# Kernel optimization log

Hardware: AMD Instinct MI355X
Metric: run time of the kernel (lower is better)

The kernel has to match this reference:

```python
import jax, jax.numpy as jnp
import numpy as np

N = 50000      # nodes
E = 800000     # edges (avg degree 16)
F_IN = 3       # dataset.num_node_features
H = 256        # hidden_channels
G = 64         # batch_size (num graphs)
OUT = 24       # lin_out output dim


def setup_inputs() -> dict:
    key = jax.random.key(0)
    ks = jax.random.split(key, 16)
    s = 0.05
    inp = {
        "x": jax.random.normal(ks[0], (N, F_IN), jnp.float32),
        "edge_index": jax.random.randint(ks[1], (2, E), 0, N, dtype=jnp.int32),
        "batch": jnp.sort(jax.random.randint(ks[2], (N,), 0, G, dtype=jnp.int32)),
        # layer 1 (F_IN -> H)
        "w_rel1": jax.random.normal(ks[3], (F_IN, H), jnp.float32) * s,
        "w_root1": jax.random.normal(ks[4], (F_IN, H), jnp.float32) * s,
        "b1": jnp.zeros((H,), jnp.float32),
        # layers 2..7 (H -> H), stacked
        "w_rel": jax.random.normal(ks[5], (6, H, H), jnp.float32) * s,
        "w_root": jax.random.normal(ks[6], (6, H, H), jnp.float32) * s,
        "b": jnp.zeros((6, H), jnp.float32),
        # output head
        "w_out": jax.random.normal(ks[7], (H, OUT), jnp.float32) * s,
        "b_out": jnp.zeros((OUT,), jnp.float32),
    }
    return inp


def reference(x, edge_index, batch, w_rel1, w_root1, b1, w_rel, w_root, b, w_out, b_out):
    src, dst = edge_index[0], edge_index[1]

    def conv(h, wr, wro, bb):
        # PyG GraphConv with add aggregation:
        # out_i = W_rel @ sum_{j -> i} h_j + b + W_root @ h_i
        agg = jax.ops.segment_sum(h[src], dst, num_segments=N)
        return agg @ wr + h @ wro + bb

    h = jax.nn.relu(conv(x, w_rel1, w_root1, b1))
    for i in range(6):
        h = jax.nn.relu(conv(h, w_rel[i], w_root[i], b[i]))

    # global_mean_pool over batch segment ids
    counts = jax.ops.segment_sum(jnp.ones((N,), h.dtype), batch, num_segments=G)
    pooled = jax.ops.segment_sum(h, batch, num_segments=G) / jnp.maximum(counts, 1.0)[:, None]

    # dropout is identity in eval mode
    return pooled @ w_out + b_out
```

## Files before the change

kernel.cpp:

```cpp
#include <hip/hip_runtime.h>

#define N_NODES 50000
#define MPAD 50048
#define N_EDGES 800000
#define H 256
#define K_CAT 512
#define G_BATCH 64
#define OUT_DIM 24

#define SCAN_BLK 256
#define NBLK ((N_NODES + SCAN_BLK - 1) / SCAN_BLK)

typedef __attribute__((ext_vector_type(8))) short short8;
typedef __attribute__((ext_vector_type(4))) float float4v;

__device__ __forceinline__ float bf2f(unsigned short u) {
    return __uint_as_float(((unsigned)u) << 16);
}
__device__ __forceinline__ unsigned short f2bf(float f) {
    unsigned x = __float_as_uint(f);
    unsigned r = (x + 0x7FFFu + ((x >> 16) & 1u)) >> 16;
    return (unsigned short)r;
}

__device__ __forceinline__ void async_copy16(void* lds, const void* g) {
    __builtin_amdgcn_global_load_lds(
        (const __attribute__((address_space(1))) unsigned int*)g,
        (__attribute__((address_space(3))) unsigned int*)lds, 16, 0, 0);
}



__global__ void histo_kernel(const int* __restrict__ dst, int* __restrict__ deg,
                             int* __restrict__ epos) {
    int e = blockIdx.x * blockDim.x + threadIdx.x;
    if (e < N_EDGES) epos[e] = atomicAdd(&deg[dst[e]], 1);
}

__global__ void scan_block(const int* __restrict__ deg, int* __restrict__ rowptr,
                           int* __restrict__ blockSums) {
    __shared__ int s[SCAN_BLK];
    int idx = blockIdx.x * SCAN_BLK + threadIdx.x;
    int v = (idx < N_NODES) ? deg[idx] : 0;
    s[threadIdx.x] = v;
    __syncthreads();
    for (int off = 1; off < SCAN_BLK; off <<= 1) {
        int t = (threadIdx.x >= off) ? s[threadIdx.x - off] : 0;
        __syncthreads();
        s[threadIdx.x] += t;
        __syncthreads();
    }
    if (idx < N_NODES) rowptr[idx] = s[threadIdx.x] - v;
    if (threadIdx.x == SCAN_BLK - 1) blockSums[blockIdx.x] = s[threadIdx.x];
}

__global__ void scan_finish(int* __restrict__ rowptr, const int* __restrict__ blockSums) {
    __shared__ int s[SCAN_BLK];
    int t = threadIdx.x;
    int v = (t < NBLK) ? blockSums[t] : 0;
    s[t] = v;
    __syncthreads();
    for (int off = 1; off < SCAN_BLK; off <<= 1) {
        int tv = (t >= off) ? s[t - off] : 0;
        __syncthreads();
        s[t] += tv;
        __syncthreads();
    }
    int prefix = (blockIdx.x > 0) ? s[blockIdx.x - 1] : 0;
    int idx = blockIdx.x * SCAN_BLK + t;
    if (idx < N_NODES) rowptr[idx] += prefix;
    if (blockIdx.x == 0 && t == 0) rowptr[N_NODES] = s[NBLK - 1];
}

__global__ void fill_csr(const int* __restrict__ src, const int* __restrict__ dst,
                         const int* __restrict__ rowptr, const int* __restrict__ epos,
                         int* __restrict__ csr_src) {
    int e = blockIdx.x * blockDim.x + threadIdx.x;
    if (e >= N_EDGES) return;
    csr_src[rowptr[dst[e]] + epos[e]] = src[e];
}


__global__ void prep_weights(const float* __restrict__ w_rel, const float* __restrict__ w_root,
                             unsigned short* __restrict__ WcatT) {
    int idx = blockIdx.x * blockDim.x + threadIdx.x;
    if (idx >= 6 * K_CAT * H) return;
    int n = idx & (H - 1);
    int k = (idx >> 8) & (K_CAT - 1);
    int l = idx >> 17;
    float v;
    if (k < H) {
        int f = (k & 0xC0) | ((k & 3) << 4) | ((k >> 2) & 15);
        v = w_rel[(size_t)l * H * H + f * H + n];
    } else {
        v = w_root[(size_t)l * H * H + (k - H) * H + n];
    }
    WcatT[(size_t)l * H * K_CAT + (size_t)n * K_CAT + k] = f2bf(v);
}


__global__ void agg3(const float* __restrict__ x, const int* __restrict__ rowptr,
                     const int* __restrict__ csr_src, float* __restrict__ agg) {
    int n = blockIdx.x * blockDim.x + threadIdx.x;
    if (n >= N_NODES) return;
    int beg = rowptr[n], end = rowptr[n + 1];
    float a0 = 0.f, a1 = 0.f, a2 = 0.f;
    for (int i = beg; i < end; ++i) {
        int s = csr_src[i];
        a0 += x[s * 3 + 0];
        a1 += x[s * 3 + 1];
        a2 += x[s * 3 + 2];
    }
    agg[n * 3 + 0] = a0;
    agg[n * 3 + 1] = a1;
    agg[n * 3 + 2] = a2;
}

__global__ void layer1_kernel(const float* __restrict__ x, const float* __restrict__ agg,
                              const float* __restrict__ wr, const float* __restrict__ wro,
                              const float* __restrict__ bias, unsigned short* __restrict__ cat,
                              unsigned char* __restrict__ h8, float* __restrict__ hscale) {
    __shared__ unsigned char tmp[H];
    int n = blockIdx.x;
    int f = threadIdx.x;
    float a0 = agg[n * 3 + 0], a1 = agg[n * 3 + 1], a2 = agg[n * 3 + 2];
    float x0 = x[n * 3 + 0], x1 = x[n * 3 + 1], x2 = x[n * 3 + 2];
    float v = bias[f];
    v += a0 * wr[0 * H + f] + a1 * wr[1 * H + f] + a2 * wr[2 * H + f];
    v += x0 * wro[0 * H + f] + x1 * wro[1 * H + f] + x2 * wro[2 * H + f];
    v = fmaxf(v, 0.f);
    cat[(size_t)n * K_CAT + H + f] = f2bf(v);
    float m = v;
#pragma unroll
    for (int off = 1; off < 64; off <<= 1) m = fmaxf(m, __shfl_xor(m, off, 64));
    float inv = m > 0.f ? 255.f / m : 0.f;
    tmp[(f & 0xC0) | ((f & 15) << 2) | ((f >> 4) & 3)] = (unsigned char)(v * inv + 0.5f);
    if ((f & 63) == 0) hscale[n * 4 + (f >> 6)] = m * (1.f / 255.f);
    __syncthreads();
    if (f < 64) *(unsigned*)(h8 + (size_t)n * H + f * 4) = *(const unsigned*)(tmp + f * 4);
}


__global__ __launch_bounds__(256) void aggH(unsigned short* __restrict__ cat,
                                            const unsigned char* __restrict__ h8,
                                            const float* __restrict__ hscale,
                                            const int* __restrict__ rowptr,
                                            const int* __restrict__ csr_src) {
    int gtid = blockIdx.x * blockDim.x + threadIdx.x;
    int node = gtid >> 6;
    if (node >= N_NODES) return;
    int lane = threadIdx.x & 63;
    int sub = lane >> 4;
    int fl = lane & 15;
    int g = fl >> 2;
    int beg = rowptr[node], end = rowptr[node + 1];

    if (beg >= end) {
        if (sub == 0) {
            uint4 z = make_uint4(0, 0, 0, 0);
            unsigned short* o = cat + (size_t)node * K_CAT + fl * 16;
            *(uint4*)o = z;
            *(uint4*)(o + 8) = z;
        }
        return;
    }

    float acc[16] = {};
    const unsigned char* base = h8 + fl * 16;
    int last = end - 1;

    int ia = beg + sub;
    int ca = ia < end ? ia : last;
    int sa = csr_src[ca];
    int ib = beg + 4 + sub;
    int cb = ib < end ? ib : last;
    int sb = csr_src[cb];
    float sca = (ia < end) ? hscale[sa * 4 + g] : 0.f;
    uint4 qa = *(const uint4*)(base + (size_t)sa * H);

    for (int i = beg; i < end; i += 4) {
        int ic = i + 8 + sub;
        int cc = ic < end ? ic : last;
        int sn = csr_src[cc];
        int inb = i + 4 + sub;
        float scb = (inb < end) ? hscale[sb * 4 + g] : 0.f;
        uint4 qb = *(const uint4*)(base + (size_t)sb * H);

        float sc = sca;
        acc[0]  = fmaf((float)(qa.x & 0xffu), sc, acc[0]);
        acc[1]  = fmaf((float)((qa.x >> 8) & 0xffu), sc, acc[1]);
        acc[2]  = fmaf((float)((qa.x >> 16) & 0xffu), sc, acc[2]);
        acc[3]  = fmaf((float)(qa.x >> 24), sc, acc[3]);
        acc[4]  = fmaf((float)(qa.y & 0xffu), sc, acc[4]);
        acc[5]  = fmaf((float)((qa.y >> 8) & 0xffu), sc, acc[5]);
        acc[6]  = fmaf((float)((qa.y >> 16) & 0xffu), sc, acc[6]);
        acc[7]  = fmaf((float)(qa.y >> 24), sc, acc[7]);
        acc[8]  = fmaf((float)(qa.z & 0xffu), sc, acc[8]);
        acc[9]  = fmaf((float)((qa.z >> 8) & 0xffu), sc, acc[9]);
        acc[10] = fmaf((float)((qa.z >> 16) & 0xffu), sc, acc[10]);
        acc[11] = fmaf((float)(qa.z >> 24), sc, acc[11]);
        acc[12] = fmaf((float)(qa.w & 0xffu), sc, acc[12]);
        acc[13] = fmaf((float)((qa.w >> 8) & 0xffu), sc, acc[13]);
        acc[14] = fmaf((float)((qa.w >> 16) & 0xffu), sc, acc[14]);
        acc[15] = fmaf((float)(qa.w >> 24), sc, acc[15]);

        sa = sb; sb = sn; sca = scb; qa = qb;
    }

#pragma unroll
    for (int j = 0; j < 16; j++) {
        acc[j] += __shfl_xor(acc[j], 16, 64);
        acc[j] += __shfl_xor(acc[j], 32, 64);
    }

    if (sub == 0) {
        unsigned short* o = cat + (size_t)node * K_CAT + fl * 16;
        uint4 p0, p1;
        p0.x = (unsigned)f2bf(acc[0])  | ((unsigned)f2bf(acc[1]) << 16);
        p0.y = (unsigned)f2bf(acc[2])  | ((unsigned)f2bf(acc[3]) << 16);
        p0.z = (unsigned)f2bf(acc[4])  | ((unsigned)f2bf(acc[5]) << 16);
        p0.w = (unsigned)f2bf(acc[6])  | ((unsigned)f2bf(acc[7]) << 16);
        p1.x = (unsigned)f2bf(acc[8])  | ((unsigned)f2bf(acc[9]) << 16);
        p1.y = (unsigned)f2bf(acc[10]) | ((unsigned)f2bf(acc[11]) << 16);
        p1.z = (unsigned)f2bf(acc[12]) | ((unsigned)f2bf(acc[13]) << 16);
        p1.w = (unsigned)f2bf(acc[14]) | ((unsigned)f2bf(acc[15]) << 16);
        *(uint4*)o = p0;
        *(uint4*)(o + 8) = p1;
    }
}


#define GBM 128
#define GBN 128
#define GBK 64

__global__ __launch_bounds__(256) void gemm_mfma(
    const unsigned short* __restrict__ cat, const unsigned short* __restrict__ WcatT,
    const float* __restrict__ bias, unsigned short* __restrict__ catOut,
    unsigned char* __restrict__ h8, float* __restrict__ hscale) {
    __shared__ unsigned short sA[GBM][GBK];
    __shared__ unsigned short sB[GBN][GBK];

    const int tid = threadIdx.x;
    const int wave = tid >> 6;
    const int lane = tid & 63;
    const int quad = lane >> 4;
    const int l16 = lane & 15;
    const int wm0 = (wave & 1) * 64;
    const int wn0 = (wave >> 1) * 64;
    const int m0 = blockIdx.x * GBM;
    const int n0 = blockIdx.y * GBN;

    const int rowoff = lane >> 3;
    const int schunk = ((lane & 7) ^ rowoff) * 8;
    const unsigned short* Asrc[4];
    const unsigned short* Bsrc[4];
#pragma unroll
    for (int j = 0; j < 4; j++) {
        int q = wave * 4 + j;
        Asrc[j] = cat + (size_t)(m0 + q * 8 + rowoff) * K_CAT + schunk;
        Bsrc[j] = WcatT + (size_t)(n0 + q * 8 + rowoff) * K_CAT + schunk;
    }

    const int sw = l16 & 7;
    const int ca0 = (quad ^ sw) * 8;
    const int ca1 = ((4 + quad) ^ sw) * 8;

    float4v acc[4][4] = {};

    for (int kk = 0; kk < K_CAT; kk += GBK) {
#pragma unroll
        for (int j = 0; j < 4; j++) {
            char* da = (char*)sA + (wave * 4 + j) * 1024;
            char* db = (char*)sB + (wave * 4 + j) * 1024;
            async_copy16(da, Asrc[j] + kk);
            async_copy16(db, Bsrc[j] + kk);
        }
        __syncthreads();

        short8 a[4][2], b[4][2];
#pragma unroll
        for (int i = 0; i < 4; i++) {
            const unsigned short* ra = &sA[wm0 + i * 16 + l16][0];
            const unsigned short* rb = &sB[wn0 + i * 16 + l16][0];
            a[i][0] = *(const short8*)(ra + ca0);
            a[i][1] = *(const short8*)(ra + ca1);
            b[i][0] = *(const short8*)(rb + ca0);
            b[i][1] = *(const short8*)(rb + ca1);
        }
#pragma unroll
        for (int sub = 0; sub < 2; sub++)
#pragma unroll
            for (int mi = 0; mi < 4; mi++)
#pragma unroll
                for (int ni = 0; ni < 4; ni++)
                    acc[mi][ni] = __builtin_amdgcn_mfma_f32_16x16x32_bf16(
                        a[mi][sub], b[ni][sub], acc[mi][ni], 0, 0, 0);
        __syncthreads();
    }

    const int hb = n0 + wn0 + l16 * 4;
    const int gsc = (n0 + wn0) >> 6;
    float bcol[4];
#pragma unroll
    for (int ni = 0; ni < 4; ni++) bcol[ni] = bias[n0 + wn0 + ni * 16 + l16];

#pragma unroll
    for (int mi = 0; mi < 4; mi++) {
        int rowb = m0 + wm0 + mi * 16 + quad * 4;
#pragma unroll
        for (int r = 0; r < 4; r++) {
            int row = rowb + r;
            float v0 = fmaxf(acc[mi][0][r] + bcol[0], 0.f);
            float v1 = fmaxf(acc[mi][1][r] + bcol[1], 0.f);
            float v2 = fmaxf(acc[mi][2][r] + bcol[2], 0.f);
            float v3 = fmaxf(acc[mi][3][r] + bcol[3], 0.f);
            unsigned short* co = catOut + (size_t)row * K_CAT + H + n0 + wn0 + l16;
            co[0]  = f2bf(v0);
            co[16] = f2bf(v1);
            co[32] = f2bf(v2);
            co[48] = f2bf(v3);
            float m = fmaxf(fmaxf(v0, v1), fmaxf(v2, v3));
            m = fmaxf(m, __shfl_xor(m, 1, 64));
            m = fmaxf(m, __shfl_xor(m, 2, 64));
            m = fmaxf(m, __shfl_xor(m, 4, 64));
            m = fmaxf(m, __shfl_xor(m, 8, 64));
            float inv = m > 0.f ? 255.f / m : 0.f;
            unsigned p = (unsigned)(v0 * inv + 0.5f)
                       | ((unsigned)(v1 * inv + 0.5f) << 8)
                       | ((unsigned)(v2 * inv + 0.5f) << 16)
                       | ((unsigned)(v3 * inv + 0.5f) << 24);
            *(unsigned*)(h8 + (size_t)row * H + hb) = p;
            if (l16 == 0) hscale[row * 4 + gsc] = m * (1.f / 255.f);
        }
    }
}


__device__ __forceinline__ int lowerBound(const int* __restrict__ batch, int val) {
    int lo = 0, hi = N_NODES;
    while (lo < hi) {
        int mid = (lo + hi) >> 1;
        if (batch[mid] < val) lo = mid + 1; else hi = mid;
    }
    return lo;
}

__global__ void pool_partial(const unsigned short* __restrict__ cat, const int* __restrict__ batch,
                             float* __restrict__ pooled) {
    int g = blockIdx.x;
    int seg = blockIdx.y;
    int f = threadIdx.x;
    int start = lowerBound(batch, g);
    int end = lowerBound(batch, g + 1);
    int len = end - start;
    int s0 = start + (int)((long long)len * seg / 8);
    int s1 = start + (int)((long long)len * (seg + 1) / 8);
    float sum = 0.f;
    for (int n = s0; n < s1; ++n)
        sum += bf2f(cat[(size_t)n * K_CAT + H + f]);
    if (s1 > s0)
        atomicAdd(&pooled[g * H + f], sum);
}

__global__ void head_kernel(const float* __restrict__ pooled, const int* __restrict__ batch,
                            const float* __restrict__ w_out, const float* __restrict__ b_out,
                            float* __restrict__ out) {
    int g = blockIdx.x;
    int o = threadIdx.x;
    int start = lowerBound(batch, g);
    int end = lowerBound(batch, g + 1);
    float cnt = fmaxf((float)(end - start), 1.f);
    float sum = 0.f;
    for (int f = 0; f < H; ++f)
        sum += pooled[g * H + f] * w_out[f * OUT_DIM + o];
    out[g * OUT_DIM + o] = b_out[o] + sum / cnt;
}


extern "C" void kernel_launch(void* const* d_in, const int* in_sizes, int n_in,
                              void* d_out, int out_size, void* d_ws, size_t ws_size,
                              hipStream_t stream) {
    const float* x      = (const float*)d_in[0];
    const int*   ei     = (const int*)d_in[1];
    const int*   batch  = (const int*)d_in[2];
    const float* w_rel1 = (const float*)d_in[3];
    const float* w_root1= (const float*)d_in[4];
    const float* b1     = (const float*)d_in[5];
    const float* w_rel  = (const float*)d_in[6];
    const float* w_root = (const float*)d_in[7];
    const float* b      = (const float*)d_in[8];
    const float* w_out  = (const float*)d_in[9];
    const float* b_out  = (const float*)d_in[10];
    float* out = (float*)d_out;

    const int* src = ei;
    const int* dst = ei + N_EDGES;

    unsigned short* catA  = (unsigned short*)d_ws;
    unsigned short* catB  = catA + (size_t)MPAD * K_CAT;
    unsigned short* WcatT = catB + (size_t)MPAD * K_CAT;
    float* agg3buf = (float*)(WcatT + (size_t)6 * H * K_CAT);
    float* pooled  = agg3buf + (size_t)N_NODES * 4;
    float* hscale  = pooled + G_BATCH * H;
    int* rowptr    = (int*)(hscale + (size_t)MPAD * 4);
    int* degcur    = rowptr + (N_NODES + 1);
    int* blockSums = degcur + N_NODES;
    int* csr_src   = blockSums + SCAN_BLK;
    int* epos      = csr_src + N_EDGES;
    unsigned char* h8 = (unsigned char*)(epos + N_EDGES);

    hipMemsetAsync(degcur, 0, N_NODES * sizeof(int), stream);
    histo_kernel<<<(N_EDGES + 255) / 256, 256, 0, stream>>>(dst, degcur, epos);
    scan_block<<<NBLK, SCAN_BLK, 0, stream>>>(degcur, rowptr, blockSums);
    scan_finish<<<NBLK, SCAN_BLK, 0, stream>>>(rowptr, blockSums);
    fill_csr<<<(N_EDGES + 255) / 256, 256, 0, stream>>>(src, dst, rowptr, epos, csr_src);

    prep_weights<<<(6 * K_CAT * H + 255) / 256, 256, 0, stream>>>(w_rel, w_root, WcatT);

    agg3<<<(N_NODES + 255) / 256, 256, 0, stream>>>(x, rowptr, csr_src, agg3buf);
    layer1_kernel<<<N_NODES, H, 0, stream>>>(x, agg3buf, w_rel1, w_root1, b1, catA, h8, hscale);

    unsigned short* cur = catA;
    unsigned short* nxt = catB;
    for (int l = 0; l < 6; ++l) {
        aggH<<<(N_NODES * 64 + 255) / 256, 256, 0, stream>>>(cur, h8, hscale, rowptr, csr_src);
        dim3 grid(MPAD / GBM, H / GBN);
        gemm_mfma<<<grid, 256, 0, stream>>>(cur, WcatT + (size_t)l * H * K_CAT,
                                            b + (size_t)l * H, nxt, h8, hscale);
        unsigned short* t = cur; cur = nxt; nxt = t;
    }

    hipMemsetAsync(pooled, 0, G_BATCH * H * sizeof(float), stream);
    pool_partial<<<dim3(G_BATCH, 8), 256, 0, stream>>>(cur, batch, pooled);
    head_kernel<<<G_BATCH, OUT_DIM, 0, stream>>>(pooled, batch, w_out, b_out, out);
}
```

Baseline: 682.8 us.

## Load GEMM MFMA operands directly from global into registers with double buffering

Removes the LDS staging (global_load_lds plus barriers) in the bf16 MFMA GEMM. Each wave now loads its A/B fragments straight from global memory into registers, using two register buffers so the next K-slice load overlaps the current MFMAs. This drops syncthreads and LDS traffic, but each block reads A and B redundantly across waves, leaning on the L2 cache. Launch bounds now request 2 blocks per CU.

```diff
diff --git a/kernel.cpp b/kernel.cpp
--- a/kernel.cpp
+++ b/kernel.cpp
@@ -21,12 +21,6 @@
     unsigned x = __float_as_uint(f);
     unsigned r = (x + 0x7FFFu + ((x >> 16) & 1u)) >> 16;
     return (unsigned short)r;
-}
-
-__device__ __forceinline__ void async_copy16(void* lds, const void* g) {
-    __builtin_amdgcn_global_load_lds(
-        (const __attribute__((address_space(1))) unsigned int*)g,
-        (__attribute__((address_space(3))) unsigned int*)lds, 16, 0, 0);
 }
 
 
@@ -232,15 +226,11 @@
 
 #define GBM 128
 #define GBN 128
-#define GBK 64
-
-__global__ __launch_bounds__(256) void gemm_mfma(
+
+__global__ __launch_bounds__(256, 2) void gemm_mfma(
     const unsigned short* __restrict__ cat, const unsigned short* __restrict__ WcatT,
     const float* __restrict__ bias, unsigned short* __restrict__ catOut,
     unsigned char* __restrict__ h8, float* __restrict__ hscale) {
-    __shared__ unsigned short sA[GBM][GBK];
-    __shared__ unsigned short sB[GBN][GBK];
-
     const int tid = threadIdx.x;
     const int wave = tid >> 6;
     const int lane = tid & 63;
@@ -251,53 +241,46 @@
     const int m0 = blockIdx.x * GBM;
     const int n0 = blockIdx.y * GBN;
 
-    const int rowoff = lane >> 3;
-    const int schunk = ((lane & 7) ^ rowoff) * 8;
-    const unsigned short* Asrc[4];
-    const unsigned short* Bsrc[4];
-#pragma unroll
-    for (int j = 0; j < 4; j++) {
-        int q = wave * 4 + j;
-        Asrc[j] = cat + (size_t)(m0 + q * 8 + rowoff) * K_CAT + schunk;
-        Bsrc[j] = WcatT + (size_t)(n0 + q * 8 + rowoff) * K_CAT + schunk;
-    }
-
-    const int sw = l16 & 7;
-    const int ca0 = (quad ^ sw) * 8;
-    const int ca1 = ((4 + quad) ^ sw) * 8;
+    const unsigned short* pa[4];
+    const unsigned short* pb[4];
+#pragma unroll
+    for (int i = 0; i < 4; i++) {
+        pa[i] = cat + (size_t)(m0 + wm0 + i * 16 + l16) * K_CAT + quad * 8;
+        pb[i] = WcatT + (size_t)(n0 + wn0 + i * 16 + l16) * K_CAT + quad * 8;
+    }
 
     float4v acc[4][4] = {};
-
-    for (int kk = 0; kk < K_CAT; kk += GBK) {
-#pragma unroll
-        for (int j = 0; j < 4; j++) {
-            char* da = (char*)sA + (wave * 4 + j) * 1024;
-            char* db = (char*)sB + (wave * 4 + j) * 1024;
-            async_copy16(da, Asrc[j] + kk);
-            async_copy16(db, Bsrc[j] + kk);
+    short8 a0[4], b0[4], a1[4], b1[4];
+
+#define LOADK(A, B, koff)                                   \
+    {                                                       \
+        _Pragma("unroll") for (int i = 0; i < 4; i++) {     \
+            A[i] = *(const short8*)(pa[i] + (koff));        \
+            B[i] = *(const short8*)(pb[i] + (koff));        \
+        }                                                   \
+    }
+
+#define MFMAK(A, B)                                                         \
+    {                                                                       \
+        _Pragma("unroll") for (int mi = 0; mi < 4; mi++)                    \
+            _Pragma("unroll") for (int ni = 0; ni < 4; ni++)                \
+                acc[mi][ni] = __builtin_amdgcn_mfma_f32_16x16x32_bf16(      \
+                    A[mi], B[ni], acc[mi][ni], 0, 0, 0);                    \
+    }
+
+    LOADK(a0, b0, 0);
+#pragma unroll
+    for (int t = 0; t < 16; t++) {
+        if (t & 1) {
+            if (t < 15) LOADK(a0, b0, (t + 1) * 32);
+            MFMAK(a1, b1);
+        } else {
+            if (t < 15) LOADK(a1, b1, (t + 1) * 32);
+            MFMAK(a0, b0);
         }
-        __syncthreads();
-
-        short8 a[4][2], b[4][2];
-#pragma unroll
-        for (int i = 0; i < 4; i++) {
-            const unsigned short* ra = &sA[wm0 + i * 16 + l16][0];
-            const unsigned short* rb = &sB[wn0 + i * 16 + l16][0];
-            a[i][0] = *(const short8*)(ra + ca0);
-            a[i][1] = *(const short8*)(ra + ca1);
-            b[i][0] = *(const short8*)(rb + ca0);
-            b[i][1] = *(const short8*)(rb + ca1);
-        }
-#pragma unroll
-        for (int sub = 0; sub < 2; sub++)
-#pragma unroll
-            for (int mi = 0; mi < 4; mi++)
-#pragma unroll
-                for (int ni = 0; ni < 4; ni++)
-                    acc[mi][ni] = __builtin_amdgcn_mfma_f32_16x16x32_bf16(
-                        a[mi][sub], b[ni][sub], acc[mi][ni], 0, 0, 0);
-        __syncthreads();
-    }
+    }
+#undef LOADK
+#undef MFMAK
 
     const int hb = n0 + wn0 + l16 * 4;
     const int gsc = (n0 + wn0) >> 6;
```

New measurement: 915.9 us. +34.1%, slower.
